# Kernel tuning notes

Measured on AMD Instinct MI355X. Metric: run time of the kernel, lower is better.

Reference implementation:

```python
import jax, jax.numpy as jnp
import numpy as np
import math

# Zernike (n, m) pairs for max_rank=3, m>=0, (n-m) even -> 6 invariants
PAIRS = [(0, 0), (1, 1), (2, 0), (2, 2), (3, 1), (3, 3)]
NUM_INV = len(PAIRS)
NUM_RANKS = 3          # max_rank + 1 = 2 + 1
CH_PER_RANK = 32
BN_EPS = 1e-5


def _radial(n, m, rho):
    """Zernike radial polynomial R_nm(rho) for the fixed pair set."""
    r2 = rho * rho
    if (n, m) == (0, 0):
        return jnp.ones_like(rho)
    if (n, m) == (1, 1):
        return rho
    if (n, m) == (2, 0):
        return 2.0 * r2 - 1.0
    if (n, m) == (2, 2):
        return r2
    if (n, m) == (3, 1):
        return (3.0 * r2 - 2.0) * rho
    if (n, m) == (3, 3):
        return r2 * rho
    raise ValueError((n, m))


def _zernike_pool(f):
    """f: (N, C, H, W) -> (N, NUM_INV, C).
    Center-of-mass shifted Zernike moment magnitudes, mean-pooled over space."""
    N, C, H, W = f.shape
    lin = jnp.linspace(-1.0, 1.0, H, dtype=f.dtype)
    Y, X = jnp.meshgrid(lin, lin, indexing='ij')   # (H, W)
    eps = 1e-6
    m00 = jnp.sum(f, axis=(-2, -1), keepdims=True)
    cx = jnp.sum(f * X, axis=(-2, -1), keepdims=True) / (m00 + eps)
    cy = jnp.sum(f * Y, axis=(-2, -1), keepdims=True) / (m00 + eps)
    Xs = X - cx                                    # (N, C, H, W)
    Ys = Y - cy
    rho = jnp.sqrt(Xs * Xs + Ys * Ys + 1e-12)
    theta = jnp.arctan2(Ys, Xs)
    mask = (rho <= 1.0).astype(f.dtype)            # unit-disk support
    fm = f * mask
    outs = []
    for n, m in PAIRS:
        R = _radial(n, m, rho)
        ang = m * theta
        re = jnp.mean(fm * R * jnp.cos(ang), axis=(-2, -1))
        im = -jnp.mean(fm * R * jnp.sin(ang), axis=(-2, -1))
        scale = (n + 1) / math.pi
        outs.append(scale * jnp.sqrt(re * re + im * im + 1e-12))
    return jnp.stack(outs, axis=1)                 # (N, NUM_INV, C)


def setup_inputs() -> dict:
    key = jax.random.key(0)
    k1, k2 = jax.random.split(key)
    B, H, W = 1024, 16, 16
    C_total = NUM_RANKS * CH_PER_RANK              # 96
    feats = NUM_INV * NUM_RANKS * CH_PER_RANK      # 576
    x = jax.random.normal(k1, (B, H, W, C_total), dtype=jnp.float32)
    gamma = jnp.ones((feats,), dtype=jnp.float32)
    beta = jnp.zeros((feats,), dtype=jnp.float32)
    W_lin = jax.random.normal(k2, (10, feats), dtype=jnp.float32) * 0.05
    b_lin = jnp.zeros((10,), dtype=jnp.float32)
    return {"x": x, "gamma": gamma, "beta": beta, "W_lin": W_lin, "b_lin": b_lin}


def reference(x, gamma, beta, W_lin, b_lin):
    B, H, W, Ct = x.shape
    # unflatten last dim -> (B, H, W, ranks, cpr), permute each rank slice to NCHW
    xr = x.reshape(B, H, W, NUM_RANKS, CH_PER_RANK)
    xr = jnp.transpose(xr, (0, 3, 4, 1, 2)).reshape(B * NUM_RANKS, CH_PER_RANK, H, W)
    pooled = _zernike_pool(xr)                     # (B*ranks, ninv, cpr)
    pooled = pooled.reshape(B, NUM_RANKS * NUM_INV * CH_PER_RANK)  # rank-major flatten
    # BatchNorm1d, training-mode batch statistics (biased var)
    mu = jnp.mean(pooled, axis=0)
    var = jnp.var(pooled, axis=0)
    z = (pooled - mu) / jnp.sqrt(var + BN_EPS) * gamma + beta
    return z @ W_lin.T + b_lin                     # (B, 10)
```

## Files before the change

### kernel.cpp

```cpp
#include <hip/hip_runtime.h>
#include <math.h>

#define PI_F 3.14159265358979323846f
#define LSTR 266

template <int CTRL>
__device__ __forceinline__ float dpp_addf(float v) {
  int p = __builtin_amdgcn_update_dpp(0, __float_as_int(v), CTRL, 0xF, 0xF, true);
  return v + __int_as_float(p);
}
__device__ __forceinline__ float red16(float v) {
  v = dpp_addf<0xB1>(v);
  v = dpp_addf<0x4E>(v);
  v = dpp_addf<0x124>(v);
  v = dpp_addf<0x128>(v);
  return v;
}

__global__ __launch_bounds__(256) void zpool_kernel(const float* __restrict__ x,
                                                    float* __restrict__ pooled) {
  const int blk = blockIdx.x;
  const int b = blk / 3;
  const int rank = blk - b * 3;
  const float* __restrict__ src = x + (size_t)b * 24576 + rank * 32;

  __shared__ float lds[32 * LSTR];
  const int t = threadIdx.x;

#pragma unroll
  for (int i = 0; i < 8; ++i) {
    const int idx = t + i * 256;
    const int p = idx >> 3;
    const int c4 = (idx & 7) * 4;
    const float4 v = *reinterpret_cast<const float4*>(src + p * 96 + c4);
    lds[(c4 + 0) * LSTR + p] = v.x;
    lds[(c4 + 1) * LSTR + p] = v.y;
    lds[(c4 + 2) * LSTR + p] = v.z;
    lds[(c4 + 3) * LSTR + p] = v.w;
  }
  __syncthreads();

  const int lane = t & 63;
  const int w = t >> 6;
  const int sub = lane >> 4;
  const int sl = lane & 15;
  const float X = -1.0f + (float)sl * (2.0f / 15.0f);

#pragma unroll
  for (int g = 0; g < 2; ++g) {
    const int ch = w * 8 + g * 4 + sub;
    const float* base = &lds[ch * LSTR + sl];
    float f[16];
#pragma unroll
    for (int k = 0; k < 16; ++k) f[k] = base[16 * k];

    float s0 = 0.0f, sy = 0.0f;
#pragma unroll
    for (int k = 0; k < 16; ++k) {
      const float Y = -1.0f + (float)k * (2.0f / 15.0f);
      s0 += f[k];
      sy = fmaf(f[k], Y, sy);
    }
    float sx = X * s0;
    s0 = red16(s0); sx = red16(sx); sy = red16(sy);
    const float invm = 1.0f / (s0 + 1e-6f);
    const float cx = sx * invm;
    const float cy = sy * invm;

    const float Xs = X - cx;
    const float Xs2 = Xs * Xs;
    const float Xs3 = Xs2 * Xs;
    const float lim = 1.0f - Xs2;

    float m0 = 0.0f, m1 = 0.0f, m2 = 0.0f, m3 = 0.0f;
#pragma unroll
    for (int k = 0; k < 16; ++k) {
      const float Y = -1.0f + (float)k * (2.0f / 15.0f);
      const float Ys = Y - cy;
      const float Ys2 = Ys * Ys;
      const float gv = (Ys2 <= lim) ? f[k] : 0.0f;
      const float gy = gv * Ys;
      m0 += gv;
      m1 += gy;
      m2 = fmaf(gy, Ys, m2);
      m3 = fmaf(gy, Ys2, m3);
    }

    float S00 = m0;
    float S10 = Xs * m0;
    float S20 = Xs2 * m0;
    float S30 = Xs3 * m0;
    float S01 = m1;
    float S11 = Xs * m1;
    float S21 = Xs2 * m1;
    float S02 = m2;
    float S12 = Xs * m2;
    float S03 = m3;

    S00 = red16(S00); S10 = red16(S10); S20 = red16(S20); S30 = red16(S30);
    S01 = red16(S01); S11 = red16(S11); S21 = red16(S21);
    S02 = red16(S02); S12 = red16(S12); S03 = red16(S03);

    if (sl == 0) {
      const float a0 = S00;
      const float a1 = S10, b1 = S01;
      const float a2 = 2.0f * (S20 + S02) - S00;
      const float a3 = S20 - S02, b3 = 2.0f * S11;
      const float a4 = 3.0f * (S30 + S12) - 2.0f * S10;
      const float b4 = 3.0f * (S21 + S03) - 2.0f * S01;
      const float a5 = S30 - 3.0f * S12;
      const float b5 = 3.0f * S21 - S03;
      float* po = pooled + (size_t)b * 576 + rank * 192 + ch;
      const float INV = 1.0f / 65536.0f;
      po[0]   = (1.0f / PI_F) * sqrtf(a0 * a0 * INV + 1e-12f);
      po[32]  = (2.0f / PI_F) * sqrtf(fmaf(a1, a1, b1 * b1) * INV + 1e-12f);
      po[64]  = (3.0f / PI_F) * sqrtf(a2 * a2 * INV + 1e-12f);
      po[96]  = (3.0f / PI_F) * sqrtf(fmaf(a3, a3, b3 * b3) * INV + 1e-12f);
      po[128] = (4.0f / PI_F) * sqrtf(fmaf(a4, a4, b4 * b4) * INV + 1e-12f);
      po[160] = (4.0f / PI_F) * sqrtf(fmaf(a5, a5, b5 * b5) * INV + 1e-12f);
    }
  }
}

__global__ __launch_bounds__(256) void bn_stats_kernel(const float* __restrict__ pooled,
                                                       const float* __restrict__ gamma,
                                                       const float* __restrict__ beta,
                                                       float* __restrict__ a,
                                                       float* __restrict__ c) {
  const int f = blockIdx.x;
  const int t = threadIdx.x;
  float s = 0.0f, sq = 0.0f;
#pragma unroll
  for (int j = 0; j < 4; ++j) {
    const float v = pooled[(size_t)(t + 256 * j) * 576 + f];
    s += v;
    sq = fmaf(v, v, sq);
  }
#pragma unroll
  for (int m = 1; m < 64; m <<= 1) {
    s += __shfl_xor(s, m);
    sq += __shfl_xor(sq, m);
  }
  __shared__ float ls[8];
  const int w = t >> 6;
  if ((t & 63) == 0) { ls[w * 2] = s; ls[w * 2 + 1] = sq; }
  __syncthreads();
  if (t == 0) {
    s = ls[0] + ls[2] + ls[4] + ls[6];
    sq = ls[1] + ls[3] + ls[5] + ls[7];
    const float mean = s * (1.0f / 1024.0f);
    const float var = fmaf(-mean, mean, sq * (1.0f / 1024.0f));
    const float istd = rsqrtf(var + 1e-5f);
    const float av = gamma[f] * istd;
    a[f] = av;
    c[f] = fmaf(-mean, av, beta[f]);
  }
}

__global__ __launch_bounds__(64) void head_kernel(const float* __restrict__ pooled,
                                                  const float* __restrict__ a,
                                                  const float* __restrict__ c,
                                                  const float* __restrict__ Wl,
                                                  const float* __restrict__ bl,
                                                  float* __restrict__ out) {
  const int row = blockIdx.x;
  const int lane = threadIdx.x;
  const float* pr = pooled + (size_t)row * 576;
  float acc0 = 0, acc1 = 0, acc2 = 0, acc3 = 0, acc4 = 0;
  float acc5 = 0, acc6 = 0, acc7 = 0, acc8 = 0, acc9 = 0;
#pragma unroll
  for (int j = 0; j < 9; ++j) {
    const int k = lane + 64 * j;
    const float z = fmaf(pr[k], a[k], c[k]);
    acc0 = fmaf(z, Wl[0 * 576 + k], acc0);
    acc1 = fmaf(z, Wl[1 * 576 + k], acc1);
    acc2 = fmaf(z, Wl[2 * 576 + k], acc2);
    acc3 = fmaf(z, Wl[3 * 576 + k], acc3);
    acc4 = fmaf(z, Wl[4 * 576 + k], acc4);
    acc5 = fmaf(z, Wl[5 * 576 + k], acc5);
    acc6 = fmaf(z, Wl[6 * 576 + k], acc6);
    acc7 = fmaf(z, Wl[7 * 576 + k], acc7);
    acc8 = fmaf(z, Wl[8 * 576 + k], acc8);
    acc9 = fmaf(z, Wl[9 * 576 + k], acc9);
  }
#pragma unroll
  for (int m = 1; m < 64; m <<= 1) {
    acc0 += __shfl_xor(acc0, m); acc1 += __shfl_xor(acc1, m);
    acc2 += __shfl_xor(acc2, m); acc3 += __shfl_xor(acc3, m);
    acc4 += __shfl_xor(acc4, m); acc5 += __shfl_xor(acc5, m);
    acc6 += __shfl_xor(acc6, m); acc7 += __shfl_xor(acc7, m);
    acc8 += __shfl_xor(acc8, m); acc9 += __shfl_xor(acc9, m);
  }
  if (lane == 0) {
    float* o = out + (size_t)row * 10;
    o[0] = acc0 + bl[0]; o[1] = acc1 + bl[1]; o[2] = acc2 + bl[2];
    o[3] = acc3 + bl[3]; o[4] = acc4 + bl[4]; o[5] = acc5 + bl[5];
    o[6] = acc6 + bl[6]; o[7] = acc7 + bl[7]; o[8] = acc8 + bl[8];
    o[9] = acc9 + bl[9];
  }
}

extern "C" void kernel_launch(void* const* d_in, const int* in_sizes, int n_in,
                              void* d_out, int out_size, void* d_ws, size_t ws_size,
                              hipStream_t stream) {
  const float* x     = (const float*)d_in[0];
  const float* gamma = (const float*)d_in[1];
  const float* beta  = (const float*)d_in[2];
  const float* Wl    = (const float*)d_in[3];
  const float* bl    = (const float*)d_in[4];
  float* out = (float*)d_out;

  float* pooled = (float*)d_ws;
  float* a = pooled + 576 * 1024;
  float* c = a + 576;

  zpool_kernel<<<3072, 256, 0, stream>>>(x, pooled);
  bn_stats_kernel<<<576, 256, 0, stream>>>(pooled, gamma, beta, a, c);
  head_kernel<<<1024, 64, 0, stream>>>(pooled, a, c, Wl, bl, out);
}
```

Before: 36.18 us.

## Keep pixel data in registers and reduce Zernike moments via DPP and small LDS partials

Removes the LDS transpose staging of the 32x256 tile. Each thread now keeps float4 channel vectors for 8 pixels in registers and works on 4 channels at once. Per-block partial sums are combined across waves through small shared buffers, first for the center of mass and then for the ten moment sums. The aim is to cut the LDS write/read traffic and bank-conflict cost. In exchange it adds two extra barriers, serial finalization work on a few threads, and 4x more DPP reductions per thread.

```diff
diff --git a/kernel.cpp b/kernel.cpp
--- a/kernel.cpp
+++ b/kernel.cpp
@@ -2,18 +2,17 @@
 #include <math.h>
 
 #define PI_F 3.14159265358979323846f
-#define LSTR 266
+typedef float floatx4 __attribute__((ext_vector_type(4)));
 
 template <int CTRL>
 __device__ __forceinline__ float dpp_addf(float v) {
   int p = __builtin_amdgcn_update_dpp(0, __float_as_int(v), CTRL, 0xF, 0xF, true);
   return v + __int_as_float(p);
 }
-__device__ __forceinline__ float red16(float v) {
+__device__ __forceinline__ float red8(float v) {
   v = dpp_addf<0xB1>(v);
   v = dpp_addf<0x4E>(v);
-  v = dpp_addf<0x124>(v);
-  v = dpp_addf<0x128>(v);
+  v = dpp_addf<0x104>(v);
   return v;
 }
 
@@ -22,103 +21,137 @@
   const int blk = blockIdx.x;
   const int b = blk / 3;
   const int rank = blk - b * 3;
-  const float* __restrict__ src = x + (size_t)b * 24576 + rank * 32;
-
-  __shared__ float lds[32 * LSTR];
+  const floatx4* __restrict__ src4 =
+      reinterpret_cast<const floatx4*>(x) + (size_t)b * 6144 + rank * 8;
+
   const int t = threadIdx.x;
-
-#pragma unroll
-  for (int i = 0; i < 8; ++i) {
-    const int idx = t + i * 256;
-    const int p = idx >> 3;
-    const int c4 = (idx & 7) * 4;
-    const float4 v = *reinterpret_cast<const float4*>(src + p * 96 + c4);
-    lds[(c4 + 0) * LSTR + p] = v.x;
-    lds[(c4 + 1) * LSTR + p] = v.y;
-    lds[(c4 + 2) * LSTR + p] = v.z;
-    lds[(c4 + 3) * LSTR + p] = v.w;
-  }
-  __syncthreads();
-
   const int lane = t & 63;
   const int w = t >> 6;
-  const int sub = lane >> 4;
-  const int sl = lane & 15;
-  const float X = -1.0f + (float)sl * (2.0f / 15.0f);
-
-#pragma unroll
-  for (int g = 0; g < 2; ++g) {
-    const int ch = w * 8 + g * 4 + sub;
-    const float* base = &lds[ch * LSTR + sl];
-    float f[16];
-#pragma unroll
-    for (int k = 0; k < 16; ++k) f[k] = base[16 * k];
-
-    float s0 = 0.0f, sy = 0.0f;
-#pragma unroll
-    for (int k = 0; k < 16; ++k) {
-      const float Y = -1.0f + (float)k * (2.0f / 15.0f);
-      s0 += f[k];
-      sy = fmaf(f[k], Y, sy);
+  const int cq = lane >> 3;
+  const int s = lane & 7;
+  const int xcol = (8 * w + s) & 15;
+  const int hoff = w >> 1;
+  const float X = -1.0f + (float)xcol * (2.0f / 15.0f);
+
+  __shared__ float p1[4][8][12];
+  __shared__ float cxy[8][8];
+  __shared__ float p2[4][8][40];
+
+  floatx4 f[8];
+#pragma unroll
+  for (int i = 0; i < 8; ++i)
+    f[i] = src4[(32 * i + 8 * w + s) * 24 + cq];
+
+  floatx4 s0v = {0, 0, 0, 0}, syv = {0, 0, 0, 0};
+#pragma unroll
+  for (int i = 0; i < 8; ++i) {
+    const float Y = -1.0f + (float)(2 * i + hoff) * (2.0f / 15.0f);
+    s0v += f[i];
+    syv += f[i] * Y;
+  }
+  floatx4 sxv = s0v * X;
+#pragma unroll
+  for (int c = 0; c < 4; ++c) {
+    s0v[c] = red8(s0v[c]);
+    sxv[c] = red8(sxv[c]);
+    syv[c] = red8(syv[c]);
+  }
+  if (s == 0) {
+#pragma unroll
+    for (int c = 0; c < 4; ++c) {
+      p1[w][cq][c] = s0v[c];
+      p1[w][cq][4 + c] = sxv[c];
+      p1[w][cq][8 + c] = syv[c];
     }
-    float sx = X * s0;
-    s0 = red16(s0); sx = red16(sx); sy = red16(sy);
-    const float invm = 1.0f / (s0 + 1e-6f);
-    const float cx = sx * invm;
-    const float cy = sy * invm;
-
-    const float Xs = X - cx;
-    const float Xs2 = Xs * Xs;
-    const float Xs3 = Xs2 * Xs;
-    const float lim = 1.0f - Xs2;
-
-    float m0 = 0.0f, m1 = 0.0f, m2 = 0.0f, m3 = 0.0f;
-#pragma unroll
-    for (int k = 0; k < 16; ++k) {
-      const float Y = -1.0f + (float)k * (2.0f / 15.0f);
-      const float Ys = Y - cy;
-      const float Ys2 = Ys * Ys;
-      const float gv = (Ys2 <= lim) ? f[k] : 0.0f;
-      const float gy = gv * Ys;
-      m0 += gv;
-      m1 += gy;
-      m2 = fmaf(gy, Ys, m2);
-      m3 = fmaf(gy, Ys2, m3);
+  }
+  __syncthreads();
+  if (t < 8) {
+#pragma unroll
+    for (int c = 0; c < 4; ++c) {
+      float S0 = 0.0f, SX = 0.0f, SY = 0.0f;
+#pragma unroll
+      for (int w2 = 0; w2 < 4; ++w2) {
+        S0 += p1[w2][t][c];
+        SX += p1[w2][t][4 + c];
+        SY += p1[w2][t][8 + c];
+      }
+      const float inv = 1.0f / (S0 + 1e-6f);
+      cxy[t][c] = SX * inv;
+      cxy[t][4 + c] = SY * inv;
     }
-
-    float S00 = m0;
-    float S10 = Xs * m0;
-    float S20 = Xs2 * m0;
-    float S30 = Xs3 * m0;
-    float S01 = m1;
-    float S11 = Xs * m1;
-    float S21 = Xs2 * m1;
-    float S02 = m2;
-    float S12 = Xs * m2;
-    float S03 = m3;
-
-    S00 = red16(S00); S10 = red16(S10); S20 = red16(S20); S30 = red16(S30);
-    S01 = red16(S01); S11 = red16(S11); S21 = red16(S21);
-    S02 = red16(S02); S12 = red16(S12); S03 = red16(S03);
-
-    if (sl == 0) {
-      const float a0 = S00;
-      const float a1 = S10, b1 = S01;
-      const float a2 = 2.0f * (S20 + S02) - S00;
-      const float a3 = S20 - S02, b3 = 2.0f * S11;
-      const float a4 = 3.0f * (S30 + S12) - 2.0f * S10;
-      const float b4 = 3.0f * (S21 + S03) - 2.0f * S01;
-      const float a5 = S30 - 3.0f * S12;
-      const float b5 = 3.0f * S21 - S03;
-      float* po = pooled + (size_t)b * 576 + rank * 192 + ch;
-      const float INV = 1.0f / 65536.0f;
-      po[0]   = (1.0f / PI_F) * sqrtf(a0 * a0 * INV + 1e-12f);
-      po[32]  = (2.0f / PI_F) * sqrtf(fmaf(a1, a1, b1 * b1) * INV + 1e-12f);
-      po[64]  = (3.0f / PI_F) * sqrtf(a2 * a2 * INV + 1e-12f);
-      po[96]  = (3.0f / PI_F) * sqrtf(fmaf(a3, a3, b3 * b3) * INV + 1e-12f);
-      po[128] = (4.0f / PI_F) * sqrtf(fmaf(a4, a4, b4 * b4) * INV + 1e-12f);
-      po[160] = (4.0f / PI_F) * sqrtf(fmaf(a5, a5, b5 * b5) * INV + 1e-12f);
+  }
+  __syncthreads();
+  floatx4 cx, cy;
+#pragma unroll
+  for (int c = 0; c < 4; ++c) { cx[c] = cxy[cq][c]; cy[c] = cxy[cq][4 + c]; }
+
+  const floatx4 Xs = X - cx;
+  const floatx4 Xs2 = Xs * Xs;
+  const floatx4 Xs3 = Xs2 * Xs;
+  const floatx4 lim = 1.0f - Xs2;
+
+  floatx4 m0 = {0,0,0,0}, m1 = {0,0,0,0}, m2 = {0,0,0,0}, m3 = {0,0,0,0};
+#pragma unroll
+  for (int i = 0; i < 8; ++i) {
+    const float Y = -1.0f + (float)(2 * i + hoff) * (2.0f / 15.0f);
+    const floatx4 Ys = Y - cy;
+    const floatx4 Ys2 = Ys * Ys;
+    floatx4 g;
+#pragma unroll
+    for (int c = 0; c < 4; ++c) g[c] = (Ys2[c] <= lim[c]) ? f[i][c] : 0.0f;
+    const floatx4 gy = g * Ys;
+    m0 += g;
+    m1 += gy;
+    m2 += gy * Ys;
+    m3 += gy * Ys2;
+  }
+
+  floatx4 S[10];
+  S[0] = m0;        S[1] = Xs * m0;  S[2] = Xs2 * m0; S[3] = Xs3 * m0;
+  S[4] = m1;        S[5] = Xs * m1;  S[6] = Xs2 * m1;
+  S[7] = m2;        S[8] = Xs * m2;  S[9] = m3;
+#pragma unroll
+  for (int v = 0; v < 10; ++v)
+#pragma unroll
+    for (int c = 0; c < 4; ++c) S[v][c] = red8(S[v][c]);
+
+  if (s == 0) {
+#pragma unroll
+    for (int v = 0; v < 10; ++v)
+#pragma unroll
+      for (int c = 0; c < 4; ++c) p2[w][cq][v * 4 + c] = S[v][c];
+  }
+  __syncthreads();
+
+  if (t < 32) {
+    const int fcq = t >> 2, comp = t & 3;
+    float T[10];
+#pragma unroll
+    for (int v = 0; v < 10; ++v) {
+      float acc = 0.0f;
+#pragma unroll
+      for (int w2 = 0; w2 < 4; ++w2) acc += p2[w2][fcq][v * 4 + comp];
+      T[v] = acc;
     }
+    const float S00 = T[0], S10 = T[1], S20 = T[2], S30 = T[3];
+    const float S01 = T[4], S11 = T[5], S21 = T[6];
+    const float S02 = T[7], S12 = T[8], S03 = T[9];
+    const float a0 = S00;
+    const float a1 = S10, b1 = S01;
+    const float a2 = 2.0f * (S20 + S02) - S00;
+    const float a3 = S20 - S02, b3 = 2.0f * S11;
+    const float a4 = 3.0f * (S30 + S12) - 2.0f * S10;
+    const float b4 = 3.0f * (S21 + S03) - 2.0f * S01;
+    const float a5 = S30 - 3.0f * S12;
+    const float b5 = 3.0f * S21 - S03;
+    float* po = pooled + (size_t)b * 576 + rank * 192 + t;
+    const float INV = 1.0f / 65536.0f;
+    po[0]   = (1.0f / PI_F) * sqrtf(a0 * a0 * INV + 1e-12f);
+    po[32]  = (2.0f / PI_F) * sqrtf(fmaf(a1, a1, b1 * b1) * INV + 1e-12f);
+    po[64]  = (3.0f / PI_F) * sqrtf(a2 * a2 * INV + 1e-12f);
+    po[96]  = (3.0f / PI_F) * sqrtf(fmaf(a3, a3, b3 * b3) * INV + 1e-12f);
+    po[128] = (4.0f / PI_F) * sqrtf(fmaf(a4, a4, b4 * b4) * INV + 1e-12f);
+    po[160] = (4.0f / PI_F) * sqrtf(fmaf(a5, a5, b5 * b5) * INV + 1e-12f);
   }
 }
 
```

Result: no change. 35.81 us (-1.0%).
